# Optimization experiments

Measured on AMD Instinct MI355X. Metric: run time of the kernel, lower is better.

## Reference

```python
import jax, jax.numpy as jnp
import numpy as np

G, N, E = 16, 512, 2048        # graphs, nodes/graph, edges/graph
CN, CE = 64, 64                # node / edge feature channels
K = 3                          # Laguerre polynomial order
RATIO = 0.5
KEEP = int(np.ceil(RATIO * N)) # 256 kept nodes per graph (static)
POWER_ITERS = 64               # power iteration approximating eigsh(k=1,'LM')


def setup_inputs() -> dict:
    key = jax.random.key(0)
    ks = jax.random.split(key, 10)
    x_n = jax.random.normal(ks[0], (G * N, CN), jnp.float32)
    x_e = jax.random.normal(ks[1], (G * E, CE), jnp.float32)
    # incidence endpoints per edge, local node ids, no self loops
    u = jax.random.randint(ks[2], (G, E), 0, N)
    v = (u + 1 + jax.random.randint(ks[3], (G, E), 0, N - 1)) % N
    # node-level conv graph (global ids within per-graph blocks): both directions
    offs = (jnp.arange(G) * N)[:, None]
    src_n = jnp.concatenate([(u + offs).reshape(-1), (v + offs).reshape(-1)])
    dst_n = jnp.concatenate([(v + offs).reshape(-1), (u + offs).reshape(-1)])
    edge_weight_n = jax.random.uniform(ks[4], (src_n.shape[0],), jnp.float32)
    # edge-level conv graph (global ids within per-graph edge blocks)
    ME = 4 * E
    offs_e = (jnp.arange(G) * E)[:, None]
    src_e = (jax.random.randint(ks[5], (G, ME), 0, E) + offs_e).reshape(-1)
    dst_e = (jax.random.randint(ks[6], (G, ME), 0, E) + offs_e).reshape(-1)
    edge_weight_e = jax.random.uniform(ks[7], (src_e.shape[0],), jnp.float32)
    # HodgeLaguerreConv(C -> 1, K) weights (glorot-ish) + bias (zeros init)
    W_n = jax.random.normal(ks[8], (K, CN), jnp.float32) / np.sqrt(CN)
    b_n = jnp.zeros((1,), jnp.float32)
    W_e = jax.random.normal(ks[9], (K, CE), jnp.float32) / np.sqrt(CE)
    b_e = jnp.zeros((1,), jnp.float32)
    return dict(x_n=x_n, x_e=x_e, edge_u=u, edge_v=v,
                src_n=src_n, dst_n=dst_n, edge_weight_n=edge_weight_n,
                src_e=src_e, dst_e=dst_e, edge_weight_e=edge_weight_e,
                W_n=W_n, b_n=b_n, W_e=W_e, b_e=b_e)


def hodge_laguerre(x, src, dst, w, Wk, b):
    """HodgeLaguerreConv with out_channels=1: out = sum_k T_k(L) x @ Wk[k] + b.
    T_0 = x; T_1 = x - Lx; T_{k+1} = (-L T_k + (2k+1) T_k - k T_{k-1})/(k+1)."""
    num = x.shape[0]
    def L(z):  # scatter-add message passing: out[i] = sum_{j->i} norm * z[j]
        return jax.ops.segment_sum(w[:, None] * z[src], dst, num_segments=num)
    Tx0 = x
    out = Tx0 @ Wk[0]
    Tx1 = x - L(x)
    out = out + Tx1 @ Wk[1]
    k = 1
    for i in range(2, Wk.shape[0]):
        Tx2 = (-L(Tx1) + (2 * k + 1) * Tx1 - k * Tx0) / (k + 1)
        out = out + Tx2 @ Wk[i]
        Tx0, Tx1 = Tx1, Tx2
        k += 1
    return out + b[0]


def pool_graph(sn, se, xn, xe, u, v):
    # node score augmented by |B1| @ edge_score (abs incidence gathers both endpoints)
    aug = sn.at[u].add(se).at[v].add(se)
    perm = jnp.argsort(-aug)                    # descending sort, take top KEEP
    mask_n = jnp.zeros((N,), xn.dtype).at[perm[:KEEP]].set(1.0)
    # mask_e = |B1|^T (1 - mask_n); keep edge iff both endpoints kept (== 0)
    bad = (1.0 - mask_n[u]) + (1.0 - mask_n[v])
    keep_e = (bad == 0.0).astype(xn.dtype)
    # dense incidence B1 [N, E]: -1 at source row, +1 at target row
    cols = jnp.arange(E)
    B = jnp.zeros((N, E), xn.dtype).at[u, cols].add(-1.0).at[v, cols].add(1.0)
    Bm = B * mask_n[:, None] * keep_e[None, :]  # row/col masking (zero-padded)
    L0 = Bm @ Bm.T                              # [N, N] node Laplacian
    L1 = Bm.T @ Bm                              # [E, E] edge Laplacian
    # power iteration for lambda_max(L0) (== eigsh k=1 'LM'; zero rows keep spectrum)
    w = jnp.ones((N,), xn.dtype) / np.sqrt(N)
    for _ in range(POWER_ITERS):
        w = L0 @ w
        w = w / (jnp.linalg.norm(w) + 1e-12)
    lam = w @ (L0 @ w)
    scale = 2.0 / (lam + 1e-12)
    return xn * mask_n[:, None], L0 * scale, xe * keep_e[:, None], L1 * scale


def reference(x_n, x_e, edge_u, edge_v, src_n, dst_n, edge_weight_n,
              src_e, dst_e, edge_weight_e, W_n, b_n, W_e, b_e):
    score_n = jax.nn.sigmoid(hodge_laguerre(x_n, src_n, dst_n, edge_weight_n, W_n, b_n).reshape(-1))
    score_e = jax.nn.sigmoid(hodge_laguerre(x_e, src_e, dst_e, edge_weight_e, W_e, b_e).reshape(-1))
    xn_g = (x_n * score_n[:, None]).reshape(G, N, CN)
    xe_g = (x_e * score_e[:, None]).reshape(G, E, CE)
    sn = score_n.reshape(G, N)
    se = score_e.reshape(G, E)
    return jax.vmap(pool_graph)(sn, se, xn_g, xe_g, edge_u, edge_v)
```

## Files before the change

### kernel.cpp

```cpp
#include <hip/hip_runtime.h>
#include <math.h>

#define GG 16
#define NNODE 512
#define EEDGE 2048
#define KEEPN 256
#define PITERS 64
#define NNT 8192
#define NET 32768

typedef float vfloat4 __attribute__((ext_vector_type(4)));

#define WS_C1N 0
#define WS_C2N 8192
#define WS_BN  16384
#define WS_C1E 24576
#define WS_C2E 57344
#define WS_BE  90112
#define WS_SNW 122880
#define WS_SEW 131072
#define WS_KLIST 163840
#define WS_KCNT 196608
#define WS_SCALE 196624

#define O_XN 0
#define O_L0 524288
#define O_XE 4718592
#define O_L1 6815744

#define AC_D1N 0
#define AC_D2N 8192
#define AC_E2N 16384
#define AC_D1E 24576
#define AC_D2E 57344
#define AC_E2E 90112
#define AC_TOT4 30720

#define L04 1048576
#define ZTOT4 17825792
#define Z_MP1_LO (AC_TOT4)
#define Z_MP2_LO (AC_TOT4 + 3932160)
#define Z_POOL_LO (AC_TOT4 + 7864320)

#define DCAP 12

__global__ __launch_bounds__(512) void k_dots(
    const float* __restrict__ xn, const float* __restrict__ xe,
    const float* __restrict__ Wn, const float* __restrict__ We,
    float* __restrict__ ws, float* __restrict__ out) {
  const int tid = threadIdx.x, bid = blockIdx.x;
  if (bid >= 1024) {
    vfloat4 z = (vfloat4)(0.f);
    vfloat4* a4 = (vfloat4*)(out + O_L0);
    int base = (bid - 1024) * 512 + tid;
    #pragma unroll
    for (int k = 0; k < 4; ++k) a4[base + k * 7680] = z;
    return;
  }
  const int lane = tid & 63;
  const int wv = (bid * 512 + tid) >> 6;
  #pragma unroll
  for (int n = 0; n < 5; ++n) {
    int gw = wv + n * 8192;
    const float* x; const float* W; int row; float *c1, *c2, *bs;
    if (gw < NNT) {
      row = gw; x = xn + (size_t)row * 64; W = Wn;
      c1 = ws + WS_C1N; c2 = ws + WS_C2N; bs = ws + WS_BN;
    } else {
      row = gw - NNT;
      x = xe + (size_t)row * 64; W = We;
      c1 = ws + WS_C1E; c2 = ws + WS_C2E; bs = ws + WS_BE;
    }
    float v = x[lane];
    float r0 = v * W[lane];
    float r1 = v * W[64 + lane];
    float r2 = v * W[128 + lane];
    for (int o = 32; o; o >>= 1) {
      r0 += __shfl_xor(r0, o, 64);
      r1 += __shfl_xor(r1, o, 64);
      r2 += __shfl_xor(r2, o, 64);
    }
    if (lane == 0) { c1[row] = r1; c2[row] = r2; bs[row] = r0 + r1 + r2; }
  }
}

__global__ __launch_bounds__(512) void k_mp1(
    const int* __restrict__ src_n, const int* __restrict__ dst_n, const float* __restrict__ wn,
    const int* __restrict__ src_e, const int* __restrict__ dst_e, const float* __restrict__ we,
    const float* __restrict__ ws, float* __restrict__ out) {
  const int tid = threadIdx.x, bid = blockIdx.x;
  if (bid >= 384) {
    vfloat4 z = (vfloat4)(0.f);
    vfloat4* o4 = (vfloat4*)out;
    int base = Z_MP1_LO + (bid - 384) * 512 + tid;
    #pragma unroll
    for (int n = 0; n < 12; ++n) {
      int i = base + n * 327680;
      int f = (i < L04) ? (O_L0 / 4 + i) : (O_L1 / 4 + (i - L04));
      __builtin_nontemporal_store(z, &o4[f]);
    }
    return;
  }
  int gid = bid * 512 + tid;
  float* acc = (float*)(out + O_L0);
  if (gid < 65536) {
    int s = src_n[gid], d = dst_n[gid]; float w = wn[gid];
    atomicAdd(&acc[AC_D1N + d], w * ws[WS_C1N + s]);
    atomicAdd(&acc[AC_D2N + d], w * ws[WS_C2N + s]);
  } else {
    int e = gid - 65536;
    int s = src_e[e], d = dst_e[e]; float w = we[e];
    atomicAdd(&acc[AC_D1E + d], w * ws[WS_C1E + s]);
    atomicAdd(&acc[AC_D2E + d], w * ws[WS_C2E + s]);
  }
}

__global__ __launch_bounds__(512) void k_mp2(
    const int* __restrict__ src_n, const int* __restrict__ dst_n, const float* __restrict__ wn,
    const int* __restrict__ src_e, const int* __restrict__ dst_e, const float* __restrict__ we,
    float* __restrict__ out) {
  const int tid = threadIdx.x, bid = blockIdx.x;
  if (bid >= 384) {
    vfloat4 z = (vfloat4)(0.f);
    vfloat4* o4 = (vfloat4*)out;
    int base = Z_MP2_LO + (bid - 384) * 512 + tid;
    #pragma unroll
    for (int n = 0; n < 12; ++n) {
      int i = base + n * 327680;
      int f = (i < L04) ? (O_L0 / 4 + i) : (O_L1 / 4 + (i - L04));
      __builtin_nontemporal_store(z, &o4[f]);
    }
    return;
  }
  int gid = bid * 512 + tid;
  float* acc = (float*)(out + O_L0);
  if (gid < 65536) {
    int s = src_n[gid], d = dst_n[gid]; float w = wn[gid];
    atomicAdd(&acc[AC_E2N + d], w * acc[AC_D2N + s]);
  } else {
    int e = gid - 65536;
    int s = src_e[e], d = dst_e[e]; float w = we[e];
    atomicAdd(&acc[AC_E2E + d], w * acc[AC_D2E + s]);
  }
}

#define PM_AUG  0
#define PM_RED  512
#define PM_IWS  520
#define PM_KCP  528
#define PM_MASK 544
#define PM_DEG  1056
#define PM_OFF  1568
#define PM_SUV  2080
#define PM_ADJ  4128
#define PM_WVA  6176
#define PM_WVB  6692
#define PM_TOT  7208

#define POWER_STEP(WCUR, WNEXT, IT)                                        \
  {                                                                        \
    float tg[DCAP];                                                        \
    _Pragma("unroll")                                                      \
    for (int k = 0; k < DCAP; ++k) tg[k] = WCUR[nbr[k]];                   \
    float acc2 = (float)myDeg * WCUR[tid];                                 \
    _Pragma("unroll")                                                      \
    for (int k = 0; k < DCAP; ++k) acc2 -= tg[k];                          \
    if (ovf) for (int p = myStart + DCAP; p < myEnd; ++p)                  \
      acc2 -= WCUR[(int)adjU[p]];                                          \
    if (((IT) & 7) == 7) {                                                 \
      float sq = acc2 * acc2;                                              \
      for (int o = 32; o; o >>= 1) sq += __shfl_xor(sq, o, 64);            \
      if (lane == 0) red[wid] = sq;                                        \
      __syncthreads();                                                     \
      float tot = red[0] + red[1] + red[2] + red[3]                        \
                + red[4] + red[5] + red[6] + red[7];                       \
      WNEXT[tid] = acc2 * (1.0f / (sqrtf(tot) + 1e-12f));                  \
    } else {                                                               \
      WNEXT[tid] = acc2;                                                   \
    }                                                                      \
    __syncthreads();                                                       \
  }

__global__ __launch_bounds__(512, 2) void k_pool(
    const int* __restrict__ edge_u, const int* __restrict__ edge_v,
    const float* __restrict__ bnp, const float* __restrict__ bep,
    float* __restrict__ ws, float* __restrict__ out) {
  const int tid = threadIdx.x;
  if (blockIdx.x >= 16) {
    vfloat4 z = (vfloat4)(0.f);
    vfloat4* o4 = (vfloat4*)out;
    int base = Z_POOL_LO + (blockIdx.x - 16) * 512 + tid;
    #pragma unroll
    for (int n = 0; n < 10; ++n) {
      int i = base + n * 1048576;
      if (i < ZTOT4) {
        int f = (i < L04) ? (O_L0 / 4 + i) : (O_L1 / 4 + (i - L04));
        __builtin_nontemporal_store(z, &o4[f]);
      }
    }
    return;
  }
  __shared__ float smem[PM_TOT];
  int* smi = (int*)smem;
  float* aug = smem + PM_AUG;
  float* red = smem + PM_RED;
  int* iws   = smi + PM_IWS;
  int* kcp   = smi + PM_KCP;
  int* maskS = smi + PM_MASK;
  int* degS  = smi + PM_DEG;
  int* offS  = smi + PM_OFF;
  int* suv   = smi + PM_SUV;
  unsigned short* adjU = (unsigned short*)(smi + PM_ADJ);
  float* wvA = smem + PM_WVA;
  float* wvB = smem + PM_WVB;

  const int g = blockIdx.x;
  const int roffN = g * NNODE;
  const int roffE = g * EEDGE;
  const int lane = tid & 63, wid = tid >> 6;
  const float* acc = (const float*)(out + O_L0);
  float biasN = bnp[0], biasE = bep[0];

  float bn  = ws[WS_BN + roffN + tid];
  float nd1 = acc[AC_D1N + roffN + tid];
  float nd2 = acc[AC_D2N + roffN + tid];
  float ne2 = acc[AC_E2N + roffN + tid];
  float beR[4], d1R[4], d2R[4], e2R[4]; int uR[4], vR[4];
  #pragma unroll
  for (int n = 0; n < 4; ++n) {
    int e = roffE + tid + n * 512;
    beR[n] = ws[WS_BE + e];
    d1R[n] = acc[AC_D1E + e];
    d2R[n] = acc[AC_D2E + e];
    e2R[n] = acc[AC_E2E + e];
    uR[n] = edge_u[e];
    vR[n] = edge_v[e];
  }

  float tn = bn - nd1 - 2.0f * nd2 + 0.5f * ne2 + biasN;
  float snw_r = 1.0f / (1.0f + expf(-tn));
  aug[tid] = snw_r;
  degS[tid] = 0;
  if (tid == 0) *kcp = 0;
  __syncthreads();

  float seR[4];
  #pragma unroll
  for (int n = 0; n < 4; ++n) {
    float te = beR[n] - d1R[n] - 2.0f * d2R[n] + 0.5f * e2R[n] + biasE;
    float s = 1.0f / (1.0f + expf(-te));
    seR[n] = s;
    atomicAdd(&aug[uR[n]], s);
    atomicAdd(&aug[vR[n]], s);
  }
  __syncthreads();

  {
    float a = aug[tid];
    int r = 0;
    #pragma unroll 8
    for (int j = 0; j < NNODE; ++j) {
      float b = aug[j];
      r += (b > a) || (b == a && j < tid);
    }
    maskS[tid] = (r < KEEPN) ? 1 : 0;
  }
  __syncthreads();
  ws[WS_SNW + roffN + tid] = snw_r * (float)maskS[tid];

  int* wsi = (int*)ws;
  #pragma unroll
  for (int n = 0; n < 4; ++n) {
    int e = tid + n * 512;
    int u = uR[n], v = vR[n];
    suv[e] = u | (v << 16);
    int k = maskS[u] & maskS[v];
    ws[WS_SEW + roffE + e] = seR[n] * (float)k;
    if (k) {
      int p = atomicAdd(kcp, 1);
      wsi[WS_KLIST + roffE + p] = e;
      atomicAdd(&degS[u], 1);
      atomicAdd(&degS[v], 1);
    }
  }
  __syncthreads();
  if (tid == 0) wsi[WS_KCNT + g] = *kcp;

  int dv = degS[tid];
  int inc = dv;
  for (int o = 1; o < 64; o <<= 1) {
    int t = __shfl_up(inc, o, 64);
    if (lane >= o) inc += t;
  }
  if (lane == 63) iws[wid] = inc;
  __syncthreads();
  int base = 0;
  for (int k = 0; k < wid; ++k) base += iws[k];
  int myStart = base + inc - dv;
  offS[tid] = myStart;
  __syncthreads();

  for (int e = tid; e < EEDGE; e += 512) {
    int p2 = suv[e];
    int u = p2 & 0xffff, v = p2 >> 16;
    if (maskS[u] & maskS[v]) {
      int pu = atomicAdd(&offS[u], 1); adjU[pu] = (unsigned short)v;
      int pv = atomicAdd(&offS[v], 1); adjU[pv] = (unsigned short)u;
    }
  }
  __syncthreads();
  int myDeg = dv;
  int myEnd = myStart + myDeg;

  int nbr[DCAP];
  #pragma unroll
  for (int k = 0; k < DCAP; ++k)
    nbr[k] = (k < myDeg) ? (int)adjU[myStart + k] : NNODE;
  bool ovf = myDeg > DCAP;

  wvA[tid] = 0.04419417382415922f;
  if (tid == 0) { wvA[NNODE] = 0.f; wvB[NNODE] = 0.f; }
  __syncthreads();
  for (int it = 0; it < PITERS; it += 2) {
    POWER_STEP(wvA, wvB, it);
    POWER_STEP(wvB, wvA, it + 1);
  }
  {
    float tg[DCAP];
    #pragma unroll
    for (int k = 0; k < DCAP; ++k) tg[k] = wvA[nbr[k]];
    float wv_ = wvA[tid];
    float acc2 = (float)myDeg * wv_;
    #pragma unroll
    for (int k = 0; k < DCAP; ++k) acc2 -= tg[k];
    if (ovf) for (int p = myStart + DCAP; p < myEnd; ++p) acc2 -= wvA[(int)adjU[p]];
    float pr = wv_ * acc2;
    for (int o = 32; o; o >>= 1) pr += __shfl_xor(pr, o, 64);
    if (lane == 0) red[wid] = pr;
    __syncthreads();
    if (tid == 0) {
      float lam = red[0] + red[1] + red[2] + red[3]
                + red[4] + red[5] + red[6] + red[7];
      ws[WS_SCALE + g] = 2.0f / (lam + 1e-12f);
    }
  }
}

__global__ __launch_bounds__(256) void k_out(
    const float* __restrict__ xn, const float* __restrict__ xe,
    const int* __restrict__ edge_u, const int* __restrict__ edge_v,
    const float* __restrict__ ws, float* __restrict__ out) {
  int b = blockIdx.x, tid = threadIdx.x;
  const int* wsi = (const int*)ws;
  if (b < 512) {
    int idx = b * 256 + tid;
    int row = idx >> 4;
    float s = ws[WS_SNW + row];
    float4 x4 = ((const float4*)xn)[idx];
    ((float4*)(out + O_XN))[idx] = make_float4(x4.x * s, x4.y * s, x4.z * s, x4.w * s);
  } else if (b < 2560) {
    int idx = (b - 512) * 256 + tid;
    int row = idx >> 4;
    float s = ws[WS_SEW + row];
    float4 x4 = ((const float4*)xe)[idx];
    ((float4*)(out + O_XE))[idx] = make_float4(x4.x * s, x4.y * s, x4.z * s, x4.w * s);
  } else if (b < 2576) {
    int g = b - 2560;
    if (g == 0) {
      float4 z4 = make_float4(0.f, 0.f, 0.f, 0.f);
      float4* a4 = (float4*)(out + O_L0);
      for (int i = tid; i < AC_TOT4; i += 256) a4[i] = z4;
      __syncthreads();
    }
    int cnt = wsi[WS_KCNT + g];
    float s = ws[WS_SCALE + g];
    float* L0 = out + O_L0 + (long long)g * (NNODE * NNODE);
    const int* kl = wsi + WS_KLIST + g * EEDGE;
    const int* eu = edge_u + g * EEDGE;
    const int* ev = edge_v + g * EEDGE;
    for (int t = tid; t < cnt; t += 256) {
      int e = kl[t];
      int u = eu[e], v = ev[e];
      atomicAdd(&L0[u * NNODE + u], s);
      atomicAdd(&L0[v * NNODE + v], s);
      atomicAdd(&L0[u * NNODE + v], -s);
      atomicAdd(&L0[v * NNODE + u], -s);
    }
  } else {
    int q = b - 2576;
    int g = q >> 8, sb = q & 255;
    int cnt = wsi[WS_KCNT + g];
    float s = ws[WS_SCALE + g];
    float* L1 = out + O_L1 + (long long)g * (EEDGE * EEDGE);
    const int* kl = wsi + WS_KLIST + g * EEDGE;
    const int* eu = edge_u + g * EEDGE;
    const int* ev = edge_v + g * EEDGE;
    for (int a = sb; a < cnt; a += 256) {
      int e1 = kl[a];
      int u1 = eu[e1], v1 = ev[e1];
      long long rowoff = (long long)e1 * EEDGE;
      for (int b2 = tid; b2 < cnt; b2 += 256) {
        int e2 = kl[b2];
        int u2 = eu[e2], v2 = ev[e2];
        int val = (u1 == u2) + (v1 == v2) - (v1 == u2) - (u1 == v2);
        if (val) L1[rowoff + e2] = s * (float)val;
      }
    }
  }
}

extern "C" void kernel_launch(void* const* d_in, const int* in_sizes, int n_in,
                              void* d_out, int out_size, void* d_ws, size_t ws_size,
                              hipStream_t stream) {
  const float* x_n = (const float*)d_in[0];
  const float* x_e = (const float*)d_in[1];
  const int* edge_u = (const int*)d_in[2];
  const int* edge_v = (const int*)d_in[3];
  const int* src_n = (const int*)d_in[4];
  const int* dst_n = (const int*)d_in[5];
  const float* ew_n = (const float*)d_in[6];
  const int* src_e = (const int*)d_in[7];
  const int* dst_e = (const int*)d_in[8];
  const float* ew_e = (const float*)d_in[9];
  const float* W_n = (const float*)d_in[10];
  const float* b_n = (const float*)d_in[11];
  const float* W_e = (const float*)d_in[12];
  const float* b_e = (const float*)d_in[13];
  float* ws = (float*)d_ws;
  float* out = (float*)d_out;

  k_dots<<<1024 + 15, 512, 0, stream>>>(x_n, x_e, W_n, W_e, ws, out);
  k_mp1<<<384 + 640, 512, 0, stream>>>(src_n, dst_n, ew_n, src_e, dst_e, ew_e, ws, out);
  k_mp2<<<384 + 640, 512, 0, stream>>>(src_n, dst_n, ew_n, src_e, dst_e, ew_e, out);
  k_pool<<<16 + 2048, 512, 0, stream>>>(edge_u, edge_v, b_n, b_e, ws, out);
  k_out<<<6672, 256, 0, stream>>>(x_n, x_e, edge_u, edge_v, ws, out);
}
```

Before: 420.0 us.

## Run power iteration in a single wavefront to eliminate block barriers

The per-graph power iteration now runs entirely in wavefront 0, with each lane handling eight nodes and holding their neighbor lists in registers. Norm reductions use only wave shuffles, which removes every __syncthreads and the shared reduction buffer from the 64 iterations. The trade-off is eight times more serial LDS gather work per lane, higher register use, and the other seven waves sitting idle.

```diff
diff --git a/kernel.cpp b/kernel.cpp
--- a/kernel.cpp
+++ b/kernel.cpp
@@ -157,28 +157,32 @@
 #define PM_WVB  6692
 #define PM_TOT  7208
 
-#define POWER_STEP(WCUR, WNEXT, IT)                                        \
+#define PSTEP(WCUR, WNEXT, IT)                                             \
   {                                                                        \
-    float tg[DCAP];                                                        \
+    float accv[8];                                                         \
     _Pragma("unroll")                                                      \
-    for (int k = 0; k < DCAP; ++k) tg[k] = WCUR[nbr[k]];                   \
-    float acc2 = (float)myDeg * WCUR[tid];                                 \
-    _Pragma("unroll")                                                      \
-    for (int k = 0; k < DCAP; ++k) acc2 -= tg[k];                          \
-    if (ovf) for (int p = myStart + DCAP; p < myEnd; ++p)                  \
-      acc2 -= WCUR[(int)adjU[p]];                                          \
+    for (int j = 0; j < 8; ++j) {                                          \
+      int n = lane + 64 * j;                                               \
+      float a = (float)deg8[j] * WCUR[n];                                  \
+      _Pragma("unroll")                                                    \
+      for (int k = 0; k < DCAP; ++k) a -= WCUR[nbf[j * DCAP + k]];         \
+      if (ovf8 & (1 << j))                                                 \
+        for (int p = st8[j] + DCAP; p < st8[j] + deg8[j]; ++p)             \
+          a -= WCUR[(int)adjU[p]];                                         \
+      accv[j] = a;                                                         \
+    }                                                                      \
     if (((IT) & 7) == 7) {                                                 \
-      float sq = acc2 * acc2;                                              \
+      float sq = 0.f;                                                      \
+      _Pragma("unroll")                                                    \
+      for (int j = 0; j < 8; ++j) sq += accv[j] * accv[j];                 \
       for (int o = 32; o; o >>= 1) sq += __shfl_xor(sq, o, 64);            \
-      if (lane == 0) red[wid] = sq;                                        \
-      __syncthreads();                                                     \
-      float tot = red[0] + red[1] + red[2] + red[3]                        \
-                + red[4] + red[5] + red[6] + red[7];                       \
-      WNEXT[tid] = acc2 * (1.0f / (sqrtf(tot) + 1e-12f));                  \
+      float inv = 1.0f / (sqrtf(sq) + 1e-12f);                             \
+      _Pragma("unroll")                                                    \
+      for (int j = 0; j < 8; ++j) WNEXT[lane + 64 * j] = accv[j] * inv;    \
     } else {                                                               \
-      WNEXT[tid] = acc2;                                                   \
+      _Pragma("unroll")                                                    \
+      for (int j = 0; j < 8; ++j) WNEXT[lane + 64 * j] = accv[j];          \
     }                                                                      \
-    __syncthreads();                                                       \
   }
 
 __global__ __launch_bounds__(512, 2) void k_pool(
@@ -203,7 +207,6 @@
   __shared__ float smem[PM_TOT];
   int* smi = (int*)smem;
   float* aug = smem + PM_AUG;
-  float* red = smem + PM_RED;
   int* iws   = smi + PM_IWS;
   int* kcp   = smi + PM_KCP;
   int* maskS = smi + PM_MASK;
@@ -309,40 +312,44 @@
     }
   }
   __syncthreads();
-  int myDeg = dv;
-  int myEnd = myStart + myDeg;
-
-  int nbr[DCAP];
-  #pragma unroll
-  for (int k = 0; k < DCAP; ++k)
-    nbr[k] = (k < myDeg) ? (int)adjU[myStart + k] : NNODE;
-  bool ovf = myDeg > DCAP;
-
-  wvA[tid] = 0.04419417382415922f;
-  if (tid == 0) { wvA[NNODE] = 0.f; wvB[NNODE] = 0.f; }
-  __syncthreads();
-  for (int it = 0; it < PITERS; it += 2) {
-    POWER_STEP(wvA, wvB, it);
-    POWER_STEP(wvB, wvA, it + 1);
-  }
-  {
-    float tg[DCAP];
-    #pragma unroll
-    for (int k = 0; k < DCAP; ++k) tg[k] = wvA[nbr[k]];
-    float wv_ = wvA[tid];
-    float acc2 = (float)myDeg * wv_;
-    #pragma unroll
-    for (int k = 0; k < DCAP; ++k) acc2 -= tg[k];
-    if (ovf) for (int p = myStart + DCAP; p < myEnd; ++p) acc2 -= wvA[(int)adjU[p]];
-    float pr = wv_ * acc2;
+
+  if (wid == 0) {
+    int deg8[8], st8[8], ovf8 = 0;
+    int nbf[8 * DCAP];
+    #pragma unroll
+    for (int j = 0; j < 8; ++j) {
+      int n = lane + 64 * j;
+      int end = offS[n];
+      int dg = degS[n];
+      int st = end - dg;
+      deg8[j] = dg; st8[j] = st;
+      if (dg > DCAP) ovf8 |= (1 << j);
+      #pragma unroll
+      for (int k = 0; k < DCAP; ++k)
+        nbf[j * DCAP + k] = (k < dg) ? (int)adjU[st + k] : NNODE;
+    }
+    #pragma unroll
+    for (int j = 0; j < 8; ++j) wvA[lane + 64 * j] = 0.04419417382415922f;
+    if (lane == 0) { wvA[NNODE] = 0.f; wvB[NNODE] = 0.f; }
+
+    for (int it = 0; it < PITERS; it += 2) {
+      PSTEP(wvA, wvB, it);
+      PSTEP(wvB, wvA, it + 1);
+    }
+    float pr = 0.f;
+    #pragma unroll
+    for (int j = 0; j < 8; ++j) {
+      int n = lane + 64 * j;
+      float a = (float)deg8[j] * wvA[n];
+      #pragma unroll
+      for (int k = 0; k < DCAP; ++k) a -= wvA[nbf[j * DCAP + k]];
+      if (ovf8 & (1 << j))
+        for (int p = st8[j] + DCAP; p < st8[j] + deg8[j]; ++p)
+          a -= wvA[(int)adjU[p]];
+      pr += wvA[n] * a;
+    }
     for (int o = 32; o; o >>= 1) pr += __shfl_xor(pr, o, 64);
-    if (lane == 0) red[wid] = pr;
-    __syncthreads();
-    if (tid == 0) {
-      float lam = red[0] + red[1] + red[2] + red[3]
-                + red[4] + red[5] + red[6] + red[7];
-      ws[WS_SCALE + g] = 2.0f / (lam + 1e-12f);
-    }
+    if (lane == 0) ws[WS_SCALE + g] = 2.0f / (pr + 1e-12f);
   }
 }
 
```

After: 463.5 us. 10.4% more time.
